# Optimization experiments

Hardware: AMD Instinct MI355X
Metric: run time of the kernel (lower is better)

Reference implementation:

```python
import jax, jax.numpy as jnp
import numpy as np

D_MODEL = 1024

def setup_inputs() -> dict:
    key = jax.random.key(0)
    ks = jax.random.split(key, 7)
    x = jax.random.normal(ks[0], (4, 2048, D_MODEL), dtype=jnp.float32)
    s = 1.0 / np.sqrt(D_MODEL)
    Wq = jax.random.uniform(ks[1], (D_MODEL, D_MODEL), jnp.float32, -s, s)
    bq = jax.random.uniform(ks[2], (D_MODEL,), jnp.float32, -s, s)
    Wk = jax.random.uniform(ks[3], (D_MODEL, D_MODEL), jnp.float32, -s, s)
    bk = jax.random.uniform(ks[4], (D_MODEL,), jnp.float32, -s, s)
    Wv = jax.random.uniform(ks[5], (D_MODEL, D_MODEL), jnp.float32, -s, s)
    bv = jax.random.uniform(ks[6], (D_MODEL,), jnp.float32, -s, s)
    return {"x": x, "Wq": Wq, "bq": bq, "Wk": Wk, "bk": bk, "Wv": Wv, "bv": bv}

def reference(x, Wq, bq, Wk, bk, Wv, bv):
    # x: [B, S, D]; Linear weights stored torch-style [out, in] -> y = x @ W.T + b
    B, S, D = x.shape
    q = jnp.einsum('bsd,ed->bse', x, Wq) + bq
    k = jnp.einsum('bsd,ed->bse', x, Wk) + bk
    v = jnp.einsum('bsd,ed->bse', x, Wv) + bv
    scores = jnp.einsum('bqd,bkd->bqk', q, k) / jnp.sqrt(jnp.float32(D))
    causal = jnp.tril(jnp.ones((S, S), dtype=bool))  # True = allowed
    scores = jnp.where(causal[None], scores, -jnp.inf)
    probs = jax.nn.softmax(scores, axis=-1)
    return jnp.einsum('bqk,bkd->bqd', probs, v)
```

## Files before the change

kernel.cpp:

```cpp
#include <hip/hip_runtime.h>
#include <hip/hip_bf16.h>
#include <stdint.h>

using bf16 = __hip_bfloat16;
typedef __bf16 bf16x8 __attribute__((ext_vector_type(8)));
typedef float  f32x4  __attribute__((ext_vector_type(4)));
typedef long   i64;
typedef unsigned char u8;

#define AS1 __attribute__((address_space(1)))
#define AS3 __attribute__((address_space(3)))

__device__ __forceinline__ void async_cp16(const void* g, void* l) {
    __builtin_amdgcn_global_load_lds((const AS1 void*)g, (AS3 void*)l, 16, 0, 0);
}

__device__ __forceinline__ unsigned pk8_lo(float a, float b, unsigned old) {
    return __builtin_amdgcn_cvt_pk_fp8_f32(a, b, old, false);
}

__global__ __launch_bounds__(256, 2) void gemm_qkv(
    const bf16* __restrict__ xb,
    const bf16* __restrict__ Wqb, const bf16* __restrict__ Wkb, const bf16* __restrict__ Wvb,
    const float* __restrict__ bq, const float* __restrict__ bk, const float* __restrict__ bv,
    u8* __restrict__ Qq, u8* __restrict__ Kq, bf16* __restrict__ Vt)
{
    const int bn = blockIdx.x, bm = blockIdx.y;
    const int seg = bn >> 3, bn_loc = bn & 7;
    const bf16*  W    = seg == 0 ? Wqb : (seg == 1 ? Wkb : Wvb);
    const float* bias = seg == 0 ? bq  : (seg == 1 ? bk  : bv);

    __shared__ bf16 sA[128 * 64];
    __shared__ bf16 sB[128 * 64];

    const int tid  = threadIdx.x;
    const int wave = tid >> 6, lane = tid & 63;
    const int wm = (wave >> 1) * 64, wn = (wave & 1) * 64;
    const int quad = lane >> 4, r16 = lane & 15;

    const bf16* Ab = xb + (long)bm * 128 * 1024;
    const bf16* Bb = W  + (long)bn_loc * 128 * 1024;

    const int rl = lane >> 3;
    const int cb = (lane & 7) ^ rl;
    const bf16* gA = Ab + (long)(wave * 32 + rl) * 1024 + cb * 8;
    const bf16* gB = Bb + (long)(wave * 32 + rl) * 1024 + cb * 8;
    char* lA = (char*)sA + wave * 32 * 128;
    char* lB = (char*)sB + wave * 32 * 128;

    f32x4 acc[4][4];
    const f32x4 zero = {0.f, 0.f, 0.f, 0.f};
#pragma unroll
    for (int i = 0; i < 4; i++)
#pragma unroll
        for (int j = 0; j < 4; j++) acc[i][j] = zero;

    for (int k0 = 0; k0 < 1024; k0 += 64) {
#pragma unroll
        for (int c = 0; c < 4; c++) {
            async_cp16(gA + (long)c * 8 * 1024 + k0, lA + c * 1024);
            async_cp16(gB + (long)c * 8 * 1024 + k0, lB + c * 1024);
        }
        __syncthreads();
#pragma unroll
        for (int kk = 0; kk < 2; kk++) {
            bf16x8 af[4], bfr[4];
#pragma unroll
            for (int t = 0; t < 4; t++) {
                int row  = wm + t * 16 + r16;
                int slot = (kk * 4 + quad) ^ (row & 7);
                af[t] = *(const bf16x8*)((const char*)sA + row * 128 + slot * 16);
            }
#pragma unroll
            for (int t = 0; t < 4; t++) {
                int row  = wn + t * 16 + r16;
                int slot = (kk * 4 + quad) ^ (row & 7);
                bfr[t] = *(const bf16x8*)((const char*)sB + row * 128 + slot * 16);
            }
#pragma unroll
            for (int mt = 0; mt < 4; mt++)
#pragma unroll
                for (int nt = 0; nt < 4; nt++)
                    acc[mt][nt] = __builtin_amdgcn_mfma_f32_16x16x32_bf16(
                        af[mt], bfr[nt], acc[mt][nt], 0, 0, 0);
        }
        __syncthreads();
    }

    if (seg < 2) {
        u8* O = seg == 0 ? Qq : Kq;
#pragma unroll
        for (int mt = 0; mt < 4; mt++) {
#pragma unroll
            for (int nt = 0; nt < 4; nt++) {
                int col = bn_loc * 128 + wn + nt * 16 + r16;
                float badd = bias[col];
#pragma unroll
                for (int rg = 0; rg < 4; rg++) {
                    long token = (long)bm * 128 + wm + mt * 16 + quad * 4 + rg;
                    float v = acc[mt][nt][rg] + badd;
                    O[token * 1024 + col] = (u8)(pk8_lo(v, v, 0u) & 0xFF);
                }
            }
        }
    } else {
#pragma unroll
        for (int mt = 0; mt < 4; mt++) {
#pragma unroll
            for (int nt = 0; nt < 4; nt++) {
                int col = bn_loc * 128 + wn + nt * 16 + r16;
                float badd = bias[col];
                long token0 = (long)bm * 128 + wm + mt * 16 + quad * 4;
                union { ushort4 u; bf16 h[4]; } o;
#pragma unroll
                for (int rg = 0; rg < 4; rg++)
                    o.h[rg] = __float2bfloat16(acc[mt][nt][rg] + badd);
                *(ushort4*)&Vt[(long)col * 8192 + token0] = o.u;
            }
        }
    }
}

__global__ __launch_bounds__(256, 2) void gemm_scores(
    const u8* __restrict__ Qq, const u8* __restrict__ Kq,
    bf16* __restrict__ P, float* __restrict__ spart)
{
    const int t = blockIdx.x, bz = blockIdx.z;
    int bm = (int)((sqrtf(8.f * t + 1.f) - 1.f) * 0.5f);
    while ((bm + 1) * (bm + 2) / 2 <= t) bm++;
    while (bm * (bm + 1) / 2 > t) bm--;
    const int bn = t - bm * (bm + 1) / 2;
    const bool diag = (bn == bm);

    __shared__ u8 sA[2][128 * 128];
    __shared__ u8 sB[2][128 * 128];

    const int tid  = threadIdx.x;
    const int wave = tid >> 6, lane = tid & 63;
    const int wm = (wave >> 1) * 64, wn = (wave & 1) * 64;
    const int quad = lane >> 4, r16 = lane & 15;
    const int whalf = wave & 1;

    const u8* Ab = Qq + (long)bz * 2048 * 1024 + (long)bm * 128 * 1024;
    const u8* Bb = Kq + (long)bz * 2048 * 1024 + (long)bn * 128 * 1024;

    const int rl = lane >> 3;
    const int cb = (lane & 7) ^ rl;
    const u8* gA = Ab + (long)(wave * 32 + rl) * 1024 + cb * 16;
    const u8* gB = Bb + (long)(wave * 32 + rl) * 1024 + cb * 16;

    f32x4 acc[4][4];
    const f32x4 zero = {0.f, 0.f, 0.f, 0.f};
#pragma unroll
    for (int i = 0; i < 4; i++)
#pragma unroll
        for (int j = 0; j < 4; j++) acc[i][j] = zero;

    for (int it = 0; it < 4; ++it) {
        const int k0 = it * 256;
#pragma unroll
        for (int s = 0; s < 2; s++) {
            u8* lA = sA[s] + wave * 32 * 128;
            u8* lB = sB[s] + wave * 32 * 128;
#pragma unroll
            for (int c = 0; c < 4; c++) {
                async_cp16(gA + (long)c * 8 * 1024 + k0 + s * 128, lA + c * 1024);
                async_cp16(gB + (long)c * 8 * 1024 + k0 + s * 128, lB + c * 1024);
            }
        }
        __syncthreads();
#pragma unroll
        for (int s = 0; s < 2; s++) {
#pragma unroll
            for (int kk = 0; kk < 4; kk++) {
                const int g  = kk * 2 + (quad >> 1);
                const int hb = (quad & 1) * 8;
                i64 av[4], bv[4];
#pragma unroll
                for (int t2 = 0; t2 < 4; t2++) {
                    int row  = wm + t2 * 16 + r16;
                    int slot = g ^ (row & 7);
                    av[t2] = *(const i64*)(sA[s] + row * 128 + slot * 16 + hb);
                }
#pragma unroll
                for (int t2 = 0; t2 < 4; t2++) {
                    int row  = wn + t2 * 16 + r16;
                    int slot = g ^ (row & 7);
                    bv[t2] = *(const i64*)(sB[s] + row * 128 + slot * 16 + hb);
                }
#pragma unroll
                for (int mt = 0; mt < 4; mt++)
#pragma unroll
                    for (int nt = 0; nt < 4; nt++)
                        acc[mt][nt] = __builtin_amdgcn_mfma_f32_16x16x32_fp8_fp8(
                            av[mt], bv[nt], acc[mt][nt], 0, 0, 0);
            }
        }
        __syncthreads();
    }

    bf16* Pb = P + (long)bz * 2048 * 2048 + (long)bm * 128 * 2048 + bn * 128;
    float rowsum[4][4];
#pragma unroll
    for (int mt = 0; mt < 4; mt++)
#pragma unroll
        for (int rg = 0; rg < 4; rg++) rowsum[mt][rg] = 0.f;

#pragma unroll
    for (int mt = 0; mt < 4; mt++) {
#pragma unroll
        for (int nt = 0; nt < 4; nt++) {
            int rcol = wn + nt * 16 + r16;
#pragma unroll
            for (int rg = 0; rg < 4; rg++) {
                int rrow = wm + mt * 16 + quad * 4 + rg;
                float e = (diag && rcol > rrow)
                            ? 0.f : __expf(acc[mt][nt][rg] * 0.03125f);
                Pb[(long)rrow * 2048 + rcol] = __float2bfloat16(e);
                rowsum[mt][rg] += e;
            }
        }
    }
#pragma unroll
    for (int off = 1; off < 16; off <<= 1)
#pragma unroll
        for (int mt = 0; mt < 4; mt++)
#pragma unroll
            for (int rg = 0; rg < 4; rg++)
                rowsum[mt][rg] += __shfl_xor(rowsum[mt][rg], off);

    float* red = (float*)sA;
    if (r16 == 0) {
#pragma unroll
        for (int mt = 0; mt < 4; mt++)
#pragma unroll
            for (int rg = 0; rg < 4; rg++)
                red[whalf * 128 + wm + mt * 16 + quad * 4 + rg] = rowsum[mt][rg];
    }
    __syncthreads();
    if (tid < 128)
        spart[((long)bz * 16 + bn) * 2048 + bm * 128 + tid] = red[tid] + red[128 + tid];
}

__global__ __launch_bounds__(256, 2) void gemm_pv(
    const bf16* __restrict__ P, const bf16* __restrict__ Vt,
    const float* __restrict__ spart, float* __restrict__ out)
{
    const int bn = blockIdx.x, bm = 15 - blockIdx.y, bz = blockIdx.z;
    const int nb = bm + 1;

    __shared__ bf16 sA[2][128 * 64];
    __shared__ bf16 sB[2][128 * 64];
    __shared__ float invl[128];

    const int tid  = threadIdx.x;
    const int wave = tid >> 6, lane = tid & 63;
    const int wm = (wave >> 1) * 64, wn = (wave & 1) * 64;
    const int quad = lane >> 4, r16 = lane & 15;

    if (tid < 128) {
        long base = (long)bz * 16 * 2048 + (long)bm * 128 + tid;
        float l = 0.f;
        for (int j = 0; j < nb; j++) l += spart[base + j * 2048];
        invl[tid] = 1.f / l;
    }

    const bf16* Ab = P  + (long)bz * 2048 * 2048 + (long)bm * 128 * 2048;
    const bf16* Bb = Vt + (long)bz * 2048 + (long)bn * 128 * 8192;

    const int rl = lane >> 3;
    const int cb = (lane & 7) ^ rl;
    const bf16* gA = Ab + (long)(wave * 32 + rl) * 2048 + cb * 8;
    const bf16* gB = Bb + (long)(wave * 32 + rl) * 8192 + cb * 8;

    f32x4 acc[4][4];
    const f32x4 zero = {0.f, 0.f, 0.f, 0.f};
#pragma unroll
    for (int i = 0; i < 4; i++)
#pragma unroll
        for (int j = 0; j < 4; j++) acc[i][j] = zero;

    for (int it = 0; it < nb; ++it) {
        const int k0 = it * 128;
#pragma unroll
        for (int s = 0; s < 2; s++) {
            char* lA = (char*)sA[s] + wave * 32 * 128;
            char* lB = (char*)sB[s] + wave * 32 * 128;
#pragma unroll
            for (int c = 0; c < 4; c++) {
                async_cp16(gA + (long)c * 8 * 2048 + k0 + s * 64, lA + c * 1024);
                async_cp16(gB + (long)c * 8 * 8192 + k0 + s * 64, lB + c * 1024);
            }
        }
        __syncthreads();
#pragma unroll
        for (int s = 0; s < 2; s++) {
#pragma unroll
            for (int kk = 0; kk < 2; kk++) {
                bf16x8 af[4], bfr[4];
#pragma unroll
                for (int t = 0; t < 4; t++) {
                    int row  = wm + t * 16 + r16;
                    int slot = (kk * 4 + quad) ^ (row & 7);
                    af[t] = *(const bf16x8*)((const char*)sA[s] + row * 128 + slot * 16);
                }
#pragma unroll
                for (int t = 0; t < 4; t++) {
                    int row  = wn + t * 16 + r16;
                    int slot = (kk * 4 + quad) ^ (row & 7);
                    bfr[t] = *(const bf16x8*)((const char*)sB[s] + row * 128 + slot * 16);
                }
#pragma unroll
                for (int mt = 0; mt < 4; mt++)
#pragma unroll
                    for (int nt = 0; nt < 4; nt++)
                        acc[mt][nt] = __builtin_amdgcn_mfma_f32_16x16x32_bf16(
                            af[mt], bfr[nt], acc[mt][nt], 0, 0, 0);
            }
        }
        __syncthreads();
    }

    float* Ob = out + (long)bz * 2048 * 1024 + (long)bm * 128 * 1024 + bn * 128;
#pragma unroll
    for (int mt = 0; mt < 4; mt++) {
#pragma unroll
        for (int nt = 0; nt < 4; nt++) {
            int rcol = wn + nt * 16 + r16;
#pragma unroll
            for (int rg = 0; rg < 4; rg++) {
                int rrow = wm + mt * 16 + quad * 4 + rg;
                Ob[(long)rrow * 1024 + rcol] = acc[mt][nt][rg] * invl[rrow];
            }
        }
    }
}

__global__ __launch_bounds__(256) void cvt_all(
    const float* __restrict__ x,
    const float* __restrict__ Wq, const float* __restrict__ Wk, const float* __restrict__ Wv,
    bf16* __restrict__ xb, bf16* __restrict__ dq, bf16* __restrict__ dk, bf16* __restrict__ dv)
{
    int b = blockIdx.x;
    const float* s; bf16* d; long off;
    if (b < 8192) { s = x; d = xb; off = (long)b * 1024; }
    else {
        int w = (b - 8192) >> 10, lb = (b - 8192) & 1023;
        s = w == 0 ? Wq : (w == 1 ? Wk : Wv);
        d = w == 0 ? dq : (w == 1 ? dk : dv);
        off = (long)lb * 1024;
    }
    long i = off + threadIdx.x * 4;
    float4 v = *(const float4*)(s + i);
    union { ushort4 u; bf16 h[4]; } o;
    o.h[0] = __float2bfloat16(v.x);
    o.h[1] = __float2bfloat16(v.y);
    o.h[2] = __float2bfloat16(v.z);
    o.h[3] = __float2bfloat16(v.w);
    *(ushort4*)(d + i) = o.u;
}

extern "C" void kernel_launch(void* const* d_in, const int* in_sizes, int n_in,
                              void* d_out, int out_size, void* d_ws, size_t ws_size,
                              hipStream_t stream)
{
    (void)in_sizes; (void)n_in; (void)out_size; (void)ws_size;
    const float* x  = (const float*)d_in[0];
    const float* Wq = (const float*)d_in[1];
    const float* bq = (const float*)d_in[2];
    const float* Wk = (const float*)d_in[3];
    const float* bk = (const float*)d_in[4];
    const float* Wv = (const float*)d_in[5];
    const float* bv = (const float*)d_in[6];
    float* out = (float*)d_out;

    char* ws = (char*)d_ws;
    bf16* xb  = (bf16*)ws;  ws += (long)8192 * 1024 * 2;
    bf16* Wqb = (bf16*)ws;  ws += (long)1024 * 1024 * 2;
    bf16* Wkb = (bf16*)ws;  ws += (long)1024 * 1024 * 2;
    bf16* Wvb = (bf16*)ws;  ws += (long)1024 * 1024 * 2;
    u8*  Qq   = (u8*)ws;    ws += (long)8192 * 1024;
    u8*  Kq   = (u8*)ws;    ws += (long)8192 * 1024;
    bf16* Vt  = (bf16*)ws;  ws += (long)8192 * 1024 * 2;
    bf16* P   = (bf16*)ws;  ws += (long)4 * 2048 * 2048 * 2;
    float* spart = (float*)ws; ws += (long)4 * 16 * 2048 * 4;

    cvt_all<<<8192 + 3072, 256, 0, stream>>>(x, Wq, Wk, Wv, xb, Wqb, Wkb, Wvb);

    gemm_qkv<<<dim3(24, 64), 256, 0, stream>>>(
        xb, Wqb, Wkb, Wvb, bq, bk, bv, Qq, Kq, Vt);

    gemm_scores<<<dim3(136, 1, 4), 256, 0, stream>>>(Qq, Kq, P, spart);

    gemm_pv<<<dim3(8, 16, 4), 256, 0, stream>>>(P, Vt, spart, out);
}
```

Baseline: 224.0 us.

## Rewrite QKV projection GEMM as 256x256 tile, 8-wave, double-buffered pipelined kernel

The QKV projection GEMM moves from 128x128 tiles with 4 waves and a single LDS buffer to 256x256 tiles with 8 waves and 128 KB of dynamic LDS split into two A and two B buffers. Async global-to-LDS loads for later k-steps are interleaved with MFMA quads under explicit vmcnt waits, barriers and raised wave priority, aiming to hide load latency and raise operand reuse. Separately, the PV kernel reverses the row-block order for half the batches to balance causal work across the launch. The larger tile shrinks the grid to 384 blocks and raises register and LDS pressure, so occupancy drops.

New measurement: 225.6 us. Within noise of the previous version (+0.7%).

```diff
diff --git a/kernel.cpp b/kernel.cpp
--- a/kernel.cpp
+++ b/kernel.cpp
@@ -19,85 +19,168 @@
     return __builtin_amdgcn_cvt_pk_fp8_f32(a, b, old, false);
 }
 
-__global__ __launch_bounds__(256, 2) void gemm_qkv(
+#define BARRIER() asm volatile("s_barrier" ::: "memory")
+#define WAITV(N)  asm volatile("s_waitcnt vmcnt(" #N ")" ::: "memory")
+
+__device__ __forceinline__ void ld_bfrag(const char* lB, int wn, int quad, int r16,
+                                         bf16x8 (&bfr)[4][2])
+{
+#pragma unroll
+    for (int nt = 0; nt < 4; nt++) {
+        int row = wn + nt * 16 + r16;
+#pragma unroll
+        for (int kk = 0; kk < 2; kk++) {
+            int slot = (kk * 4 + quad) ^ (row & 7);
+            bfr[nt][kk] = *(const bf16x8*)(lB + row * 128 + slot * 16);
+        }
+    }
+}
+
+__device__ __forceinline__ void ld_afrag(const char* lA, int wm, int quad, int r16, int q,
+                                         bf16x8 (&af)[2][2])
+{
+#pragma unroll
+    for (int t = 0; t < 2; t++) {
+        int row = wm + (q * 2 + t) * 16 + r16;
+#pragma unroll
+        for (int kk = 0; kk < 2; kk++) {
+            int slot = (kk * 4 + quad) ^ (row & 7);
+            af[t][kk] = *(const bf16x8*)(lA + row * 128 + slot * 16);
+        }
+    }
+}
+
+__device__ __forceinline__ void mfma_quad(int q, bf16x8 (&af)[2][2], bf16x8 (&bfr)[4][2],
+                                          f32x4 (&acc)[8][4])
+{
+    __builtin_amdgcn_s_setprio(1);
+#pragma unroll
+    for (int mt = 0; mt < 2; mt++)
+#pragma unroll
+        for (int nt = 0; nt < 4; nt++)
+#pragma unroll
+            for (int kk = 0; kk < 2; kk++)
+                acc[q * 2 + mt][nt] = __builtin_amdgcn_mfma_f32_16x16x32_bf16(
+                    af[mt][kk], bfr[nt][kk], acc[q * 2 + mt][nt], 0, 0, 0);
+    __builtin_amdgcn_s_setprio(0);
+}
+
+__global__ __launch_bounds__(512, 2) void gemm_qkv(
     const bf16* __restrict__ xb,
     const bf16* __restrict__ Wqb, const bf16* __restrict__ Wkb, const bf16* __restrict__ Wvb,
     const float* __restrict__ bq, const float* __restrict__ bk, const float* __restrict__ bv,
     u8* __restrict__ Qq, u8* __restrict__ Kq, bf16* __restrict__ Vt)
 {
+    extern __shared__ char smem[];
     const int bn = blockIdx.x, bm = blockIdx.y;
-    const int seg = bn >> 3, bn_loc = bn & 7;
+    const int seg = bn >> 2, bn_loc = bn & 3;
     const bf16*  W    = seg == 0 ? Wqb : (seg == 1 ? Wkb : Wvb);
     const float* bias = seg == 0 ? bq  : (seg == 1 ? bk  : bv);
 
-    __shared__ bf16 sA[128 * 64];
-    __shared__ bf16 sB[128 * 64];
-
     const int tid  = threadIdx.x;
     const int wave = tid >> 6, lane = tid & 63;
-    const int wm = (wave >> 1) * 64, wn = (wave & 1) * 64;
+    const int wm = (wave >> 2) * 128, wn = (wave & 3) * 64;
     const int quad = lane >> 4, r16 = lane & 15;
 
-    const bf16* Ab = xb + (long)bm * 128 * 1024;
-    const bf16* Bb = W  + (long)bn_loc * 128 * 1024;
-
-    const int rl = lane >> 3;
-    const int cb = (lane & 7) ^ rl;
-    const bf16* gA = Ab + (long)(wave * 32 + rl) * 1024 + cb * 8;
-    const bf16* gB = Bb + (long)(wave * 32 + rl) * 1024 + cb * 8;
-    char* lA = (char*)sA + wave * 32 * 128;
-    char* lB = (char*)sB + wave * 32 * 128;
-
-    f32x4 acc[4][4];
+    char* A0 = smem;
+    char* A1 = smem + 32768;
+    char* B0 = smem + 65536;
+    char* B1 = smem + 98304;
+
+    const bf16* Ab = xb + (long)bm * 256 * 1024;
+    const bf16* Bb = W  + (long)bn_loc * 256 * 1024;
+
+    const int rl  = lane >> 3;
+    const int cbg = (lane & 7) ^ rl;
+    const bf16* gA = Ab + (long)(wave * 32 + rl) * 1024 + cbg * 8;
+    const bf16* gB = Bb + (long)(wave * 32 + rl) * 1024 + cbg * 8;
+    const int woff = wave * 4096;
+
+    auto stage = [&](char* dst, const bf16* src, int k0, int c) {
+        async_cp16(src + (long)c * 8192 + k0, dst + woff + c * 1024);
+    };
+
+    f32x4 acc[8][4];
     const f32x4 zero = {0.f, 0.f, 0.f, 0.f};
 #pragma unroll
-    for (int i = 0; i < 4; i++)
+    for (int i = 0; i < 8; i++)
 #pragma unroll
         for (int j = 0; j < 4; j++) acc[i][j] = zero;
 
-    for (int k0 = 0; k0 < 1024; k0 += 64) {
-#pragma unroll
-        for (int c = 0; c < 4; c++) {
-            async_cp16(gA + (long)c * 8 * 1024 + k0, lA + c * 1024);
-            async_cp16(gB + (long)c * 8 * 1024 + k0, lB + c * 1024);
-        }
-        __syncthreads();
-#pragma unroll
-        for (int kk = 0; kk < 2; kk++) {
-            bf16x8 af[4], bfr[4];
-#pragma unroll
-            for (int t = 0; t < 4; t++) {
-                int row  = wm + t * 16 + r16;
-                int slot = (kk * 4 + quad) ^ (row & 7);
-                af[t] = *(const bf16x8*)((const char*)sA + row * 128 + slot * 16);
-            }
-#pragma unroll
-            for (int t = 0; t < 4; t++) {
-                int row  = wn + t * 16 + r16;
-                int slot = (kk * 4 + quad) ^ (row & 7);
-                bfr[t] = *(const bf16x8*)((const char*)sB + row * 128 + slot * 16);
-            }
-#pragma unroll
-            for (int mt = 0; mt < 4; mt++)
-#pragma unroll
-                for (int nt = 0; nt < 4; nt++)
-                    acc[mt][nt] = __builtin_amdgcn_mfma_f32_16x16x32_bf16(
-                        af[mt], bfr[nt], acc[mt][nt], 0, 0, 0);
-        }
-        __syncthreads();
+#pragma unroll
+    for (int c = 0; c < 4; c++) stage(B0, gB, 0, c);
+#pragma unroll
+    for (int c = 0; c < 4; c++) stage(A0, gA, 0, c);
+#pragma unroll
+    for (int c = 0; c < 4; c++) stage(B1, gB, 64, c);
+    stage(A1, gA, 64, 0); stage(A1, gA, 64, 1);
+    WAITV(6);
+    BARRIER();
+
+    bf16x8 bfr[4][2], af[2][2];
+#pragma unroll 1
+    for (int i = 0; i < 8; ++i) {
+        const int kO  = i * 128 + 64;
+        const int kE2 = i * 128 + 128;
+        const int kO2 = i * 128 + 192;
+        const bool pre = (i < 7);
+
+        ld_bfrag(B0, wn, quad, r16, bfr);
+        ld_afrag(A0, wm, quad, r16, 0, af);
+        stage(A1, gA, kO, 2); stage(A1, gA, kO, 3);
+        BARRIER();
+        mfma_quad(0, af, bfr, acc);
+        BARRIER();
+        ld_afrag(A0, wm, quad, r16, 1, af);
+        if (pre) { stage(B0, gB, kE2, 0); stage(B0, gB, kE2, 1); }
+        BARRIER();
+        mfma_quad(1, af, bfr, acc);
+        BARRIER();
+        ld_afrag(A0, wm, quad, r16, 2, af);
+        if (pre) { stage(B0, gB, kE2, 2); stage(B0, gB, kE2, 3); }
+        BARRIER();
+        mfma_quad(2, af, bfr, acc);
+        BARRIER();
+        ld_afrag(A0, wm, quad, r16, 3, af);
+        if (pre) { stage(A0, gA, kE2, 0); stage(A0, gA, kE2, 1); WAITV(6); }
+        else     { WAITV(0); }
+        BARRIER();
+        mfma_quad(3, af, bfr, acc);
+        BARRIER();
+        ld_bfrag(B1, wn, quad, r16, bfr);
+        ld_afrag(A1, wm, quad, r16, 0, af);
+        if (pre) { stage(A0, gA, kE2, 2); stage(A0, gA, kE2, 3); }
+        BARRIER();
+        mfma_quad(0, af, bfr, acc);
+        BARRIER();
+        ld_afrag(A1, wm, quad, r16, 1, af);
+        if (pre) { stage(B1, gB, kO2, 0); stage(B1, gB, kO2, 1); }
+        BARRIER();
+        mfma_quad(1, af, bfr, acc);
+        BARRIER();
+        ld_afrag(A1, wm, quad, r16, 2, af);
+        if (pre) { stage(B1, gB, kO2, 2); stage(B1, gB, kO2, 3); }
+        BARRIER();
+        mfma_quad(2, af, bfr, acc);
+        BARRIER();
+        ld_afrag(A1, wm, quad, r16, 3, af);
+        if (pre) { stage(A1, gA, kO2, 0); stage(A1, gA, kO2, 1); WAITV(6); }
+        BARRIER();
+        mfma_quad(3, af, bfr, acc);
+        BARRIER();
     }
 
     if (seg < 2) {
         u8* O = seg == 0 ? Qq : Kq;
 #pragma unroll
-        for (int mt = 0; mt < 4; mt++) {
+        for (int mt = 0; mt < 8; mt++) {
 #pragma unroll
             for (int nt = 0; nt < 4; nt++) {
-                int col = bn_loc * 128 + wn + nt * 16 + r16;
+                int col = bn_loc * 256 + wn + nt * 16 + r16;
                 float badd = bias[col];
 #pragma unroll
                 for (int rg = 0; rg < 4; rg++) {
-                    long token = (long)bm * 128 + wm + mt * 16 + quad * 4 + rg;
+                    long token = (long)bm * 256 + wm + mt * 16 + quad * 4 + rg;
                     float v = acc[mt][nt][rg] + badd;
                     O[token * 1024 + col] = (u8)(pk8_lo(v, v, 0u) & 0xFF);
                 }
@@ -105,12 +188,12 @@
         }
     } else {
 #pragma unroll
-        for (int mt = 0; mt < 4; mt++) {
+        for (int mt = 0; mt < 8; mt++) {
 #pragma unroll
             for (int nt = 0; nt < 4; nt++) {
-                int col = bn_loc * 128 + wn + nt * 16 + r16;
+                int col = bn_loc * 256 + wn + nt * 16 + r16;
                 float badd = bias[col];
-                long token0 = (long)bm * 128 + wm + mt * 16 + quad * 4;
+                long token0 = (long)bm * 256 + wm + mt * 16 + quad * 4;
                 union { ushort4 u; bf16 h[4]; } o;
 #pragma unroll
                 for (int rg = 0; rg < 4; rg++)
@@ -246,7 +329,8 @@
     const bf16* __restrict__ P, const bf16* __restrict__ Vt,
     const float* __restrict__ spart, float* __restrict__ out)
 {
-    const int bn = blockIdx.x, bm = 15 - blockIdx.y, bz = blockIdx.z;
+    const int bn = blockIdx.x, by = blockIdx.y, bz = blockIdx.z;
+    const int bm = (bz < 2) ? (15 - by) : by;
     const int nb = bm + 1;
 
     __shared__ bf16 sA[2][128 * 64];
@@ -385,9 +469,16 @@
     bf16* P   = (bf16*)ws;  ws += (long)4 * 2048 * 2048 * 2;
     float* spart = (float*)ws; ws += (long)4 * 16 * 2048 * 4;
 
+    static bool attr_set = false;
+    if (!attr_set) {
+        hipFuncSetAttribute(reinterpret_cast<const void*>(gemm_qkv),
+                            hipFuncAttributeMaxDynamicSharedMemorySize, 131072);
+        attr_set = true;
+    }
+
     cvt_all<<<8192 + 3072, 256, 0, stream>>>(x, Wq, Wk, Wv, xb, Wqb, Wkb, Wvb);
 
-    gemm_qkv<<<dim3(24, 64), 256, 0, stream>>>(
+    gemm_qkv<<<dim3(12, 32), 512, 131072, stream>>>(
         xb, Wqb, Wkb, Wvb, bq, bk, bv, Qq, Kq, Vt);
 
     gemm_scores<<<dim3(136, 1, 4), 256, 0, stream>>>(Qq, Kq, P, spart);
```

## Stage GEMM epilogues through LDS for coalesced stores and remap blocks per XCD

Applied to the files above, without the earlier changes.

The QKV, scores and PV kernels now write their output tiles into a shared-memory staging buffer with padded or swizzled rows. Each tile is then written out with wide 8- or 16-byte coalesced global stores, replacing the scattered per-element byte and bf16 stores. The scores and PV kernels also remap the block index so neighbouring tiles land on the same XCD, aiming for better L2 locality; PV alternates the bm ordering per batch. This costs an extra LDS round trip and a barrier, and the scores kernel's larger shared buffer may affect occupancy.

After: 214.6 us. -4.2%, faster.

```diff
diff --git a/kernel.cpp b/kernel.cpp
--- a/kernel.cpp
+++ b/kernel.cpp
@@ -5,8 +5,10 @@
 using bf16 = __hip_bfloat16;
 typedef __bf16 bf16x8 __attribute__((ext_vector_type(8)));
 typedef float  f32x4  __attribute__((ext_vector_type(4)));
+typedef int    i32x4  __attribute__((ext_vector_type(4)));
 typedef long   i64;
 typedef unsigned char u8;
+typedef unsigned long long u64;
 
 #define AS1 __attribute__((address_space(1)))
 #define AS3 __attribute__((address_space(3)))
@@ -25,18 +27,17 @@
     const float* __restrict__ bq, const float* __restrict__ bk, const float* __restrict__ bv,
     u8* __restrict__ Qq, u8* __restrict__ Kq, bf16* __restrict__ Vt)
 {
+    __shared__ char qsm[32768];
     const int bn = blockIdx.x, bm = blockIdx.y;
     const int seg = bn >> 3, bn_loc = bn & 7;
     const bf16*  W    = seg == 0 ? Wqb : (seg == 1 ? Wkb : Wvb);
     const float* bias = seg == 0 ? bq  : (seg == 1 ? bk  : bv);
 
-    __shared__ bf16 sA[128 * 64];
-    __shared__ bf16 sB[128 * 64];
-
     const int tid  = threadIdx.x;
     const int wave = tid >> 6, lane = tid & 63;
     const int wm = (wave >> 1) * 64, wn = (wave & 1) * 64;
     const int quad = lane >> 4, r16 = lane & 15;
+    const int lane16 = r16;
 
     const bf16* Ab = xb + (long)bm * 128 * 1024;
     const bf16* Bb = W  + (long)bn_loc * 128 * 1024;
@@ -45,8 +46,8 @@
     const int cb = (lane & 7) ^ rl;
     const bf16* gA = Ab + (long)(wave * 32 + rl) * 1024 + cb * 8;
     const bf16* gB = Bb + (long)(wave * 32 + rl) * 1024 + cb * 8;
-    char* lA = (char*)sA + wave * 32 * 128;
-    char* lB = (char*)sB + wave * 32 * 128;
+    char* lA = qsm         + wave * 32 * 128;
+    char* lB = qsm + 16384 + wave * 32 * 128;
 
     f32x4 acc[4][4];
     const f32x4 zero = {0.f, 0.f, 0.f, 0.f};
@@ -69,13 +70,13 @@
             for (int t = 0; t < 4; t++) {
                 int row  = wm + t * 16 + r16;
                 int slot = (kk * 4 + quad) ^ (row & 7);
-                af[t] = *(const bf16x8*)((const char*)sA + row * 128 + slot * 16);
+                af[t] = *(const bf16x8*)(qsm + row * 128 + slot * 16);
             }
 #pragma unroll
             for (int t = 0; t < 4; t++) {
                 int row  = wn + t * 16 + r16;
                 int slot = (kk * 4 + quad) ^ (row & 7);
-                bfr[t] = *(const bf16x8*)((const char*)sB + row * 128 + slot * 16);
+                bfr[t] = *(const bf16x8*)(qsm + 16384 + row * 128 + slot * 16);
             }
 #pragma unroll
             for (int mt = 0; mt < 4; mt++)
@@ -93,30 +94,45 @@
         for (int mt = 0; mt < 4; mt++) {
 #pragma unroll
             for (int nt = 0; nt < 4; nt++) {
-                int col = bn_loc * 128 + wn + nt * 16 + r16;
-                float badd = bias[col];
+                int lcol = wn + nt * 16 + r16;
+                float badd = bias[bn_loc * 128 + lcol];
 #pragma unroll
                 for (int rg = 0; rg < 4; rg++) {
-                    long token = (long)bm * 128 + wm + mt * 16 + quad * 4 + rg;
+                    int lrow = wm + mt * 16 + quad * 4 + rg;
                     float v = acc[mt][nt][rg] + badd;
-                    O[token * 1024 + col] = (u8)(pk8_lo(v, v, 0u) & 0xFF);
+                    qsm[lrow * 136 + lcol] = (u8)(pk8_lo(v, v, 0u) & 0xFF);
                 }
             }
         }
+        __syncthreads();
+#pragma unroll
+        for (int j = 0; j < 8; j++) {
+            int lrow = (tid >> 4) + j * 16;
+            u64 v = *(const u64*)(qsm + lrow * 136 + lane16 * 8);
+            *(u64*)&O[((long)bm * 128 + lrow) * 1024 + bn_loc * 128 + lane16 * 8] = v;
+        }
     } else {
 #pragma unroll
         for (int mt = 0; mt < 4; mt++) {
 #pragma unroll
             for (int nt = 0; nt < 4; nt++) {
-                int col = bn_loc * 128 + wn + nt * 16 + r16;
-                float badd = bias[col];
-                long token0 = (long)bm * 128 + wm + mt * 16 + quad * 4;
+                int lcol = wn + nt * 16 + r16;
+                float badd = bias[bn_loc * 128 + lcol];
                 union { ushort4 u; bf16 h[4]; } o;
 #pragma unroll
                 for (int rg = 0; rg < 4; rg++)
                     o.h[rg] = __float2bfloat16(acc[mt][nt][rg] + badd);
-                *(ushort4*)&Vt[(long)col * 8192 + token0] = o.u;
-            }
+                int g16 = ((wm >> 3) + mt * 2 + (quad >> 1)) ^ (lcol & 7);
+                *(ushort4*)(qsm + lcol * 256 + g16 * 16 + (quad & 1) * 8) = o.u;
+            }
+        }
+        __syncthreads();
+#pragma unroll
+        for (int j = 0; j < 8; j++) {
+            int lcol = (tid >> 4) + j * 16;
+            int g = lane16 ^ (lcol & 7);
+            i32x4 v = *(const i32x4*)(qsm + lcol * 256 + g * 16);
+            *(i32x4*)&Vt[((long)bn_loc * 128 + lcol) * 8192 + (long)bm * 128 + lane16 * 8] = v;
         }
     }
 }
@@ -125,20 +141,21 @@
     const u8* __restrict__ Qq, const u8* __restrict__ Kq,
     bf16* __restrict__ P, float* __restrict__ spart)
 {
-    const int t = blockIdx.x, bz = blockIdx.z;
+    __shared__ char ssm[65536];
+    const int lin = blockIdx.x + 136 * blockIdx.z;
+    const int ntg = (lin & 7) * 68 + (lin >> 3);
+    const int t = ntg % 136, bz = ntg / 136;
     int bm = (int)((sqrtf(8.f * t + 1.f) - 1.f) * 0.5f);
     while ((bm + 1) * (bm + 2) / 2 <= t) bm++;
     while (bm * (bm + 1) / 2 > t) bm--;
     const int bn = t - bm * (bm + 1) / 2;
     const bool diag = (bn == bm);
 
-    __shared__ u8 sA[2][128 * 128];
-    __shared__ u8 sB[2][128 * 128];
-
     const int tid  = threadIdx.x;
     const int wave = tid >> 6, lane = tid & 63;
     const int wm = (wave >> 1) * 64, wn = (wave & 1) * 64;
     const int quad = lane >> 4, r16 = lane & 15;
+    const int lane16 = r16;
     const int whalf = wave & 1;
 
     const u8* Ab = Qq + (long)bz * 2048 * 1024 + (long)bm * 128 * 1024;
@@ -160,8 +177,8 @@
         const int k0 = it * 256;
 #pragma unroll
         for (int s = 0; s < 2; s++) {
-            u8* lA = sA[s] + wave * 32 * 128;
-            u8* lB = sB[s] + wave * 32 * 128;
+            char* lA = ssm + s * 16384         + wave * 32 * 128;
+            char* lB = ssm + 32768 + s * 16384 + wave * 32 * 128;
 #pragma unroll
             for (int c = 0; c < 4; c++) {
                 async_cp16(gA + (long)c * 8 * 1024 + k0 + s * 128, lA + c * 1024);
@@ -180,13 +197,13 @@
                 for (int t2 = 0; t2 < 4; t2++) {
                     int row  = wm + t2 * 16 + r16;
                     int slot = g ^ (row & 7);
-                    av[t2] = *(const i64*)(sA[s] + row * 128 + slot * 16 + hb);
+                    av[t2] = *(const i64*)(ssm + s * 16384 + row * 128 + slot * 16 + hb);
                 }
 #pragma unroll
                 for (int t2 = 0; t2 < 4; t2++) {
                     int row  = wn + t2 * 16 + r16;
                     int slot = g ^ (row & 7);
-                    bv[t2] = *(const i64*)(sB[s] + row * 128 + slot * 16 + hb);
+                    bv[t2] = *(const i64*)(ssm + 32768 + s * 16384 + row * 128 + slot * 16 + hb);
                 }
 #pragma unroll
                 for (int mt = 0; mt < 4; mt++)
@@ -199,7 +216,6 @@
         __syncthreads();
     }
 
-    bf16* Pb = P + (long)bz * 2048 * 2048 + (long)bm * 128 * 2048 + bn * 128;
     float rowsum[4][4];
 #pragma unroll
     for (int mt = 0; mt < 4; mt++)
@@ -216,7 +232,7 @@
                 int rrow = wm + mt * 16 + quad * 4 + rg;
                 float e = (diag && rcol > rrow)
                             ? 0.f : __expf(acc[mt][nt][rg] * 0.03125f);
-                Pb[(long)rrow * 2048 + rcol] = __float2bfloat16(e);
+                *(bf16*)(ssm + rrow * 272 + rcol * 2) = __float2bfloat16(e);
                 rowsum[mt][rg] += e;
             }
         }
@@ -229,7 +245,7 @@
             for (int rg = 0; rg < 4; rg++)
                 rowsum[mt][rg] += __shfl_xor(rowsum[mt][rg], off);
 
-    float* red = (float*)sA;
+    float* red = (float*)(ssm + 34816);
     if (r16 == 0) {
 #pragma unroll
         for (int mt = 0; mt < 4; mt++)
@@ -240,14 +256,28 @@
     __syncthreads();
     if (tid < 128)
         spart[((long)bz * 16 + bn) * 2048 + bm * 128 + tid] = red[tid] + red[128 + tid];
+
+    bf16* Pb = P + (long)bz * 2048 * 2048 + (long)bm * 128 * 2048 + bn * 128;
+#pragma unroll
+    for (int j = 0; j < 8; j++) {
+        int prow = (tid >> 4) + j * 16;
+        i32x4 v = *(const i32x4*)(ssm + prow * 272 + lane16 * 16);
+        *(i32x4*)&Pb[(long)prow * 2048 + lane16 * 8] = v;
+    }
 }
 
 __global__ __launch_bounds__(256, 2) void gemm_pv(
     const bf16* __restrict__ P, const bf16* __restrict__ Vt,
     const float* __restrict__ spart, float* __restrict__ out)
 {
-    const int bn = blockIdx.x, bm = 15 - blockIdx.y, bz = blockIdx.z;
-    const int nb = bm + 1;
+    const int lin = blockIdx.x + 8 * blockIdx.y + 128 * blockIdx.z;
+    const int xcd = lin & 7;
+    const int m   = lin >> 3;
+    const int bn  = m & 7;
+    const int g   = xcd + 8 * (m >> 3);
+    const int by  = g & 15, bz = g >> 4;
+    const int bm  = (bz < 2) ? (15 - by) : by;
+    const int nb  = bm + 1;
 
     __shared__ bf16 sA[2][128 * 64];
     __shared__ bf16 sB[2][128 * 64];
```
